# Optimization experiments

Measured on AMD Instinct MI355X. Metric: run time of the kernel, lower is better.

## Reference

```python
import jax, jax.numpy as jnp
import numpy as np

QMIN, QMAX = -128, 127  # 8-bit symmetric
EPS = 1e-8

def _fake_quant(v, scale, axis):
    # per-channel symmetric fake quant: round, clamp, dequant
    shape = [1] * v.ndim
    shape[axis] = -1
    s = (jnp.abs(scale) + EPS).reshape(shape)
    q = jnp.clip(jnp.round(v / s), QMIN, QMAX)
    return q * s

def setup_inputs() -> dict:
    key = jax.random.key(0)
    k1, k2, k3, k4, k5 = jax.random.split(key, 5)
    B, C_in, L = 32, 512, 4096
    C_out, K = 512, 3
    return {
        "x": jax.random.normal(k1, (B, C_in, L), dtype=jnp.float32),
        "weight": jax.random.normal(k2, (C_out, C_in, K), dtype=jnp.float32) * 0.05,
        "bias": jax.random.normal(k3, (C_out,), dtype=jnp.float32) * 0.1,
        "a_scale": jax.random.uniform(k4, (C_in,), dtype=jnp.float32, minval=0.01, maxval=0.1),
        "w_scale": jax.random.uniform(k5, (C_out,), dtype=jnp.float32, minval=0.001, maxval=0.01),
    }

def reference(x, weight, bias, a_scale, w_scale):
    # activations: per-channel (axis=1 of NCL) symmetric int8 fake-quant
    x_hat = _fake_quant(x, a_scale, axis=1)
    # weights: per-out-channel (axis=0 of OIK) symmetric int8 fake-quant
    w_hat = _fake_quant(weight, w_scale, axis=0)
    out = jax.lax.conv_general_dilated(
        x_hat, w_hat,
        window_strides=(1,), padding=[(1, 1)], rhs_dilation=(1,),
        dimension_numbers=("NCH", "OIH", "NCH"))
    return out + bias[None, :, None]
```

## Files before the change

### kernel.cpp

```cpp
#include <hip/hip_runtime.h>
#include <hip/hip_bf16.h>
#include <stdint.h>

#define BATCH 32
#define CIN   512
#define LLEN  4096
#define COUT  512
#define KW    3
#define KTOT  (CIN * KW)
#define LPAD  (LLEN + 2)
#define EPSQ  1e-8f

typedef __bf16 bf16x8 __attribute__((ext_vector_type(8)));
typedef float  floatx4 __attribute__((ext_vector_type(4)));

__device__ __forceinline__ void async_load16(const void* gptr, void* ldsptr) {
    __builtin_amdgcn_global_load_lds(
        (const __attribute__((address_space(1))) void*)gptr,
        (__attribute__((address_space(3))) void*)ldsptr,
        16, 0, 0);
}

__global__ void zero_pad_kernel(uint32_t* __restrict__ qxT_u32) {
    int idx = blockIdx.x * blockDim.x + threadIdx.x;
    int b = idx >> 9;
    int r = (idx >> 8) & 1;
    int c = idx & 255;
    size_t row = (size_t)b * LPAD + (r ? (LPAD - 1) : 0);
    qxT_u32[row * (CIN / 2) + c] = 0u;
}

__global__ __launch_bounds__(256) void quantx_kernel(
        const float* __restrict__ x,
        const float* __restrict__ a_scale,
        __bf16* __restrict__ qxT) {
    __shared__ __bf16 qs[64][66];
    const int i0 = blockIdx.x * 64;
    const int l0 = blockIdx.y * 64;
    const int b  = blockIdx.z;
    const int tid = threadIdx.x;

    const int f4   = tid & 15;
    const int irow = tid >> 4;
    #pragma unroll
    for (int p = 0; p < 4; ++p) {
        int i = p * 16 + irow;
        float s = fabsf(a_scale[i0 + i]) + EPSQ;
        float inv = 1.0f / s;
        const floatx4* xrow = (const floatx4*)(x + ((size_t)(b * CIN + i0 + i)) * LLEN + l0);
        floatx4 v = xrow[f4];
        #pragma unroll
        for (int j = 0; j < 4; ++j) {
            float q = fminf(fmaxf(rintf(v[j] * inv), -128.0f), 127.0f);
            qs[f4 * 4 + j][i] = (__bf16)q;
        }
    }
    __syncthreads();

    const int c4 = tid & 15;
    const int rr = tid >> 4;
    uint2* outp = (uint2*)(qxT + ((size_t)b * LPAD + (l0 + 1)) * CIN + i0);
    #pragma unroll
    for (int p = 0; p < 4; ++p) {
        int l = p * 16 + rr;
        const uint32_t* qrow = (const uint32_t*)&qs[l][0];
        uint2 u;
        u.x = qrow[2 * c4];
        u.y = qrow[2 * c4 + 1];
        outp[(size_t)l * (CIN / 4) + c4] = u;
    }
}

__global__ void wfold_kernel(
        const float* __restrict__ w,
        const float* __restrict__ a_scale,
        const float* __restrict__ w_scale,
        __bf16* __restrict__ Wf) {
    int idx = blockIdx.x * blockDim.x + threadIdx.x;
    if (idx >= COUT * KTOT) return;
    int o   = idx / KTOT;
    int rem = idx - o * KTOT;
    int k = rem >> 9;
    int i = rem & 511;
    float sw = fabsf(w_scale[o]) + EPSQ;
    float sa = fabsf(a_scale[i]) + EPSQ;
    float q = fminf(fmaxf(rintf(w[((size_t)o * CIN + i) * KW + k] / sw), -128.0f), 127.0f);
    Wf[idx] = (__bf16)(q * sa * sw);
}

__global__ __launch_bounds__(256) void qconv_gemm(
        const __bf16* __restrict__ Wf,
        const __bf16* __restrict__ qxT,
        const float* __restrict__ bias,
        float* __restrict__ out) {
    __shared__ __attribute__((aligned(16))) __bf16 Asmem[128 * 64];
    __shared__ __attribute__((aligned(16))) __bf16 Bsmem[128 * 64];

    const int tid  = threadIdx.x;
    const int m0   = blockIdx.x * 128;
    const int l0   = blockIdx.y * 128;
    const int b    = blockIdx.z;
    const int wave = tid >> 6;
    const int lane = tid & 63;
    const int wm = wave >> 1, wn = wave & 1;
    const int row16 = lane & 15;
    const int quad  = lane >> 4;

    floatx4 acc[4][4];
    #pragma unroll
    for (int i = 0; i < 4; ++i)
        #pragma unroll
        for (int j = 0; j < 4; ++j)
            acc[i][j] = (floatx4){0.f, 0.f, 0.f, 0.f};

    const __bf16* qxb = qxT + (size_t)b * LPAD * CIN;

    for (int t = 0; t < KTOT / 64; ++t) {
        const int kk0  = t * 64;
        const int kblk = kk0 >> 9;
        const int i0   = kk0 & 511;

        #pragma unroll
        for (int j = 0; j < 4; ++j) {
            int chunk = j * 256 + tid;
            int arow  = chunk >> 3;
            int gcol  = (chunk & 7) ^ (arow & 7);
            async_load16(Wf + (size_t)(m0 + arow) * KTOT + kk0 + gcol * 8,
                         (char*)Asmem + chunk * 16);
        }
        #pragma unroll
        for (int j = 0; j < 4; ++j) {
            int chunk = j * 256 + tid;
            int brow  = chunk >> 3;
            int gcol  = (chunk & 7) ^ (brow & 7);
            async_load16(qxb + (size_t)(l0 + brow + kblk) * CIN + i0 + gcol * 8,
                         (char*)Bsmem + chunk * 16);
        }
        __syncthreads();

        #pragma unroll
        for (int ks = 0; ks < 2; ++ks) {
            bf16x8 afrag[4], bfrag[4];
            #pragma unroll
            for (int mt = 0; mt < 4; ++mt) {
                int arow = wm * 64 + mt * 16 + row16;
                int js   = (ks * 4 + quad) ^ (arow & 7);
                afrag[mt] = *(const bf16x8*)(Asmem + arow * 64 + js * 8);
            }
            #pragma unroll
            for (int nt = 0; nt < 4; ++nt) {
                int brow = wn * 64 + nt * 16 + row16;
                int js   = (ks * 4 + quad) ^ (brow & 7);
                bfrag[nt] = *(const bf16x8*)(Bsmem + brow * 64 + js * 8);
            }
            #pragma unroll
            for (int mt = 0; mt < 4; ++mt)
                #pragma unroll
                for (int nt = 0; nt < 4; ++nt)
                    acc[mt][nt] = __builtin_amdgcn_mfma_f32_16x16x32_bf16(
                        afrag[mt], bfrag[nt], acc[mt][nt], 0, 0, 0);
        }
        __syncthreads();
    }

    float* outb = out + (size_t)b * COUT * LLEN;
    #pragma unroll
    for (int mt = 0; mt < 4; ++mt) {
        #pragma unroll
        for (int r = 0; r < 4; ++r) {
            int o = m0 + wm * 64 + mt * 16 + quad * 4 + r;
            float bv = bias[o];
            #pragma unroll
            for (int nt = 0; nt < 4; ++nt) {
                int l = l0 + wn * 64 + nt * 16 + row16;
                outb[(size_t)o * LLEN + l] = acc[mt][nt][r] + bv;
            }
        }
    }
}

extern "C" void kernel_launch(void* const* d_in, const int* in_sizes, int n_in,
                              void* d_out, int out_size, void* d_ws, size_t ws_size,
                              hipStream_t stream) {
    const float* x       = (const float*)d_in[0];
    const float* weight  = (const float*)d_in[1];
    const float* bias    = (const float*)d_in[2];
    const float* a_scale = (const float*)d_in[3];
    const float* w_scale = (const float*)d_in[4];
    float* out = (float*)d_out;

    __bf16* Wf  = (__bf16*)d_ws;
    __bf16* qxT = (__bf16*)((char*)d_ws + (size_t)COUT * KTOT * sizeof(__bf16));

    wfold_kernel<<<dim3((COUT * KTOT) / 256), dim3(256), 0, stream>>>(
        weight, a_scale, w_scale, Wf);
    zero_pad_kernel<<<dim3(64), dim3(256), 0, stream>>>((uint32_t*)qxT);
    quantx_kernel<<<dim3(CIN / 64, LLEN / 64, BATCH), dim3(256), 0, stream>>>(
        x, a_scale, qxT);
    qconv_gemm<<<dim3(COUT / 128, LLEN / 128, BATCH), dim3(256), 0, stream>>>(
        Wf, qxT, bias, out);
}
```

Before: 718.5 us.

## Restructure conv GEMM into 256x256 tiles with 4-stage async LDS pipeline

Grows the GEMM block tile to 256x256 with 512 threads and 8 waves, and shrinks BK to 32. Global-to-LDS loads now run through a 4-slot ring with three stages prefetched, using explicit vmcnt waits instead of a load-then-sync each step. It also remaps block IDs into an XCD-aware order so neighbouring tiles share cache, and raises wave priority around the MFMA block. The goal is to hide memory latency and raise reuse per loaded byte, at the cost of more registers (128 accumulators per lane), 128KB of LDS, and fewer blocks in the grid.

After: 712.0 us. No clear change (-0.9%).

```diff
diff --git a/kernel.cpp b/kernel.cpp
--- a/kernel.cpp
+++ b/kernel.cpp
@@ -10,6 +10,12 @@
 #define KTOT  (CIN * KW)
 #define LPAD  (LLEN + 2)
 #define EPSQ  1e-8f
+
+#define BM 256
+#define BN 256
+#define BK 32
+#define NT (KTOT / BK)
+#define TILE_ELEMS (BM * BK)
 
 typedef __bf16 bf16x8 __attribute__((ext_vector_type(8)));
 typedef float  floatx4 __attribute__((ext_vector_type(4)));
@@ -88,88 +94,113 @@
     Wf[idx] = (__bf16)(q * sa * sw);
 }
 
-__global__ __launch_bounds__(256) void qconv_gemm(
+__global__ __launch_bounds__(512, 2) void qconv_gemm(
         const __bf16* __restrict__ Wf,
         const __bf16* __restrict__ qxT,
         const float* __restrict__ bias,
         float* __restrict__ out) {
-    __shared__ __attribute__((aligned(16))) __bf16 Asmem[128 * 64];
-    __shared__ __attribute__((aligned(16))) __bf16 Bsmem[128 * 64];
-
-    const int tid  = threadIdx.x;
-    const int m0   = blockIdx.x * 128;
-    const int l0   = blockIdx.y * 128;
-    const int b    = blockIdx.z;
-    const int wave = tid >> 6;
-    const int lane = tid & 63;
-    const int wm = wave >> 1, wn = wave & 1;
+    __shared__ __attribute__((aligned(16))) __bf16 As[4][TILE_ELEMS];
+    __shared__ __attribute__((aligned(16))) __bf16 Bs[4][TILE_ELEMS];
+
+    const int tid = threadIdx.x;
+
+    int flat = blockIdx.x + gridDim.x * (blockIdx.y + gridDim.y * blockIdx.z);
+    int logical = (flat & 7) * 128 + (flat >> 3);
+    const int m0 = (logical & 1) * BM;
+    const int l0 = ((logical >> 1) & 15) * BN;
+    const int b  = logical >> 5;
+
+    const int wave  = tid >> 6;
+    const int lane  = tid & 63;
+    const int wm    = wave >> 2;
+    const int wn    = wave & 3;
     const int row16 = lane & 15;
     const int quad  = lane >> 4;
 
-    floatx4 acc[4][4];
-    #pragma unroll
-    for (int i = 0; i < 4; ++i)
-        #pragma unroll
-        for (int j = 0; j < 4; ++j)
-            acc[i][j] = (floatx4){0.f, 0.f, 0.f, 0.f};
-
     const __bf16* qxb = qxT + (size_t)b * LPAD * CIN;
 
-    for (int t = 0; t < KTOT / 64; ++t) {
-        const int kk0  = t * 64;
+    floatx4 acc[8][4];
+    #pragma unroll
+    for (int mt = 0; mt < 8; ++mt)
+        #pragma unroll
+        for (int nt = 0; nt < 4; ++nt)
+            acc[mt][nt] = (floatx4){0.f, 0.f, 0.f, 0.f};
+
+    const int ca0 = tid,        ca1 = 512 + tid;
+    const int ra0 = ca0 >> 2,   ra1 = ca1 >> 2;
+    const int ga0 = (ca0 & 3) ^ (ra0 & 3);
+    const int ga1 = (ca1 & 3) ^ (ra1 & 3);
+    const __bf16* aptr0 = Wf  + (size_t)(m0 + ra0) * KTOT + ga0 * 8;
+    const __bf16* aptr1 = Wf  + (size_t)(m0 + ra1) * KTOT + ga1 * 8;
+    const __bf16* bptr0 = qxb + (size_t)(l0 + ra0) * CIN  + ga0 * 8;
+    const __bf16* bptr1 = qxb + (size_t)(l0 + ra1) * CIN  + ga1 * 8;
+
+    auto STAGE = [&](int t) {
+        const int kk0  = t * BK;
         const int kblk = kk0 >> 9;
         const int i0   = kk0 & 511;
-
-        #pragma unroll
-        for (int j = 0; j < 4; ++j) {
-            int chunk = j * 256 + tid;
-            int arow  = chunk >> 3;
-            int gcol  = (chunk & 7) ^ (arow & 7);
-            async_load16(Wf + (size_t)(m0 + arow) * KTOT + kk0 + gcol * 8,
-                         (char*)Asmem + chunk * 16);
-        }
-        #pragma unroll
-        for (int j = 0; j < 4; ++j) {
-            int chunk = j * 256 + tid;
-            int brow  = chunk >> 3;
-            int gcol  = (chunk & 7) ^ (brow & 7);
-            async_load16(qxb + (size_t)(l0 + brow + kblk) * CIN + i0 + gcol * 8,
-                         (char*)Bsmem + chunk * 16);
-        }
-        __syncthreads();
-
-        #pragma unroll
-        for (int ks = 0; ks < 2; ++ks) {
-            bf16x8 afrag[4], bfrag[4];
+        const int slot = t & 3;
+        char* abase = (char*)&As[slot][0];
+        char* bbase = (char*)&Bs[slot][0];
+        async_load16(aptr0 + kk0,                        abase + ca0 * 16);
+        async_load16(aptr1 + kk0,                        abase + ca1 * 16);
+        async_load16(bptr0 + (size_t)kblk * CIN + i0,    bbase + ca0 * 16);
+        async_load16(bptr1 + (size_t)kblk * CIN + i0,    bbase + ca1 * 16);
+    };
+
+    STAGE(0); STAGE(1); STAGE(2);
+
+    for (int t = 0; t < NT; ++t) {
+        __builtin_amdgcn_sched_barrier(0);
+        __builtin_amdgcn_s_barrier();
+        __builtin_amdgcn_sched_barrier(0);
+
+        if (t + 3 < NT) STAGE(t + 3);
+
+        if (t < NT - 3)      asm volatile("s_waitcnt vmcnt(12)" ::: "memory");
+        else if (t == NT-3)  asm volatile("s_waitcnt vmcnt(8)"  ::: "memory");
+        else if (t == NT-2)  asm volatile("s_waitcnt vmcnt(4)"  ::: "memory");
+        else                 asm volatile("s_waitcnt vmcnt(0)"  ::: "memory");
+
+        __builtin_amdgcn_sched_barrier(0);
+        __builtin_amdgcn_s_barrier();
+        __builtin_amdgcn_sched_barrier(0);
+
+        const int slot = t & 3;
+        const __bf16* Ab = &As[slot][0];
+        const __bf16* Bb = &Bs[slot][0];
+
+        bf16x8 af[8], bfr[4];
+        #pragma unroll
+        for (int mt = 0; mt < 8; ++mt) {
+            int arow = wm * 128 + mt * 16 + row16;
+            int js   = quad ^ (arow & 3);
+            af[mt] = *(const bf16x8*)(Ab + arow * BK + js * 8);
+        }
+        #pragma unroll
+        for (int nt = 0; nt < 4; ++nt) {
+            int brow = wn * 64 + nt * 16 + row16;
+            int js   = quad ^ (brow & 3);
+            bfr[nt] = *(const bf16x8*)(Bb + brow * BK + js * 8);
+        }
+
+        __builtin_amdgcn_s_setprio(1);
+        #pragma unroll
+        for (int mt = 0; mt < 8; ++mt)
             #pragma unroll
-            for (int mt = 0; mt < 4; ++mt) {
-                int arow = wm * 64 + mt * 16 + row16;
-                int js   = (ks * 4 + quad) ^ (arow & 7);
-                afrag[mt] = *(const bf16x8*)(Asmem + arow * 64 + js * 8);
-            }
-            #pragma unroll
-            for (int nt = 0; nt < 4; ++nt) {
-                int brow = wn * 64 + nt * 16 + row16;
-                int js   = (ks * 4 + quad) ^ (brow & 7);
-                bfrag[nt] = *(const bf16x8*)(Bsmem + brow * 64 + js * 8);
-            }
-            #pragma unroll
-            for (int mt = 0; mt < 4; ++mt)
-                #pragma unroll
-                for (int nt = 0; nt < 4; ++nt)
-                    acc[mt][nt] = __builtin_amdgcn_mfma_f32_16x16x32_bf16(
-                        afrag[mt], bfrag[nt], acc[mt][nt], 0, 0, 0);
-        }
-        __syncthreads();
-    }
-
-    float* outb = out + (size_t)b * COUT * LLEN;
-    #pragma unroll
-    for (int mt = 0; mt < 4; ++mt) {
+            for (int nt = 0; nt < 4; ++nt)
+                acc[mt][nt] = __builtin_amdgcn_mfma_f32_16x16x32_bf16(
+                    af[mt], bfr[nt], acc[mt][nt], 0, 0, 0);
+        __builtin_amdgcn_s_setprio(0);
+    }
+
+    float* outb = out + ((size_t)b * COUT + m0) * LLEN;
+    #pragma unroll
+    for (int mt = 0; mt < 8; ++mt) {
         #pragma unroll
         for (int r = 0; r < 4; ++r) {
-            int o = m0 + wm * 64 + mt * 16 + quad * 4 + r;
-            float bv = bias[o];
+            int o = wm * 128 + mt * 16 + quad * 4 + r;
+            float bv = bias[m0 + o];
             #pragma unroll
             for (int nt = 0; nt < 4; ++nt) {
                 int l = l0 + wn * 64 + nt * 16 + row16;
@@ -197,6 +228,6 @@
     zero_pad_kernel<<<dim3(64), dim3(256), 0, stream>>>((uint32_t*)qxT);
     quantx_kernel<<<dim3(CIN / 64, LLEN / 64, BATCH), dim3(256), 0, stream>>>(
         x, a_scale, qxT);
-    qconv_gemm<<<dim3(COUT / 128, LLEN / 128, BATCH), dim3(256), 0, stream>>>(
+    qconv_gemm<<<dim3(COUT / BM, LLEN / BN, BATCH), dim3(512), 0, stream>>>(
         Wf, qxT, bias, out);
 }
```
